# Optimization experiments

Measured on AMD Instinct MI355X. Metric: run time of the kernel, lower is better.

## Reference

```python
import jax, jax.numpy as jnp
import numpy as np

EPS = 1e-5
C = 64  # in_channels == feat_channels == out_channels


def _ln(x, g, b):
    m = jnp.mean(x, axis=-1, keepdims=True)
    v = jnp.mean(jnp.square(x - m), axis=-1, keepdims=True)
    return (x - m) * jax.lax.rsqrt(v + EPS) * g + b


def setup_inputs() -> dict:
    key = jax.random.key(0)
    ks = jax.random.split(key, 10)
    bs, nc, H, W = 8, 80, 256, 256
    d = {
        "feat": jax.random.normal(ks[0], (bs, C, H, W), jnp.float32),
        "head": jax.random.normal(ks[1], (bs, nc, C, 1), jnp.float32),
        "pred": jax.random.normal(ks[2], (bs, nc, H // 2, W // 2), jnp.float32),
        # linear transforms (stored [in, out], applied as x @ W + b)
        "W_pred_t": jax.random.normal(ks[3], (C, 2 * C), jnp.float32) * 0.05,
        "b_pred_t": jnp.zeros((2 * C,), jnp.float32),
        "W_head_t": jax.random.normal(ks[4], (C, 2 * C), jnp.float32) * 0.05,
        "b_head_t": jnp.zeros((2 * C,), jnp.float32),
        "W_pred_g": jax.random.normal(ks[5], (C, C), jnp.float32) * 0.05,
        "b_pred_g": jnp.zeros((C,), jnp.float32),
        "W_head_g": jax.random.normal(ks[6], (C, C), jnp.float32) * 0.05,
        "b_head_g": jnp.zeros((C,), jnp.float32),
        "W_fc": jax.random.normal(ks[7], (C, C), jnp.float32) * 0.05,
        "b_fc": jnp.zeros((C,), jnp.float32),
        # layernorm params
        "g_pin": jnp.ones((C,), jnp.float32), "be_pin": jnp.zeros((C,), jnp.float32),
        "g_hin": jnp.ones((C,), jnp.float32), "be_hin": jnp.zeros((C,), jnp.float32),
        "g_pout": jnp.ones((C,), jnp.float32), "be_pout": jnp.zeros((C,), jnp.float32),
        "g_hout": jnp.ones((C,), jnp.float32), "be_hout": jnp.zeros((C,), jnp.float32),
        "g_fc": jnp.ones((C,), jnp.float32), "be_fc": jnp.zeros((C,), jnp.float32),
    }
    return d


def reference(feat, head, pred,
              W_pred_t, b_pred_t, W_head_t, b_head_t,
              W_pred_g, b_pred_g, W_head_g, b_head_g,
              W_fc, b_fc,
              g_pin, be_pin, g_hin, be_hin,
              g_pout, be_pout, g_hout, be_hout,
              g_fc, be_fc):
    bs, nc = head.shape[:2]
    H, W = feat.shape[2], feat.shape[3]
    pred_up = jax.image.resize(pred, (bs, nc, H, W), method="bilinear")
    pred_up = jax.nn.sigmoid(pred_up)
    # head-aware feature assembly: [bs, nc, C]
    assemble = jnp.einsum("bnhw,bchw->bnc", pred_up, feat)
    a = assemble.reshape(-1, C)                      # [BN, C]
    BN = a.shape[0]
    # head: [bs, nc, C, kk] -> [BN, kk, C]
    hd = jnp.transpose(head.reshape(bs, nc, C, -1), (0, 1, 3, 2)).reshape(BN, -1, C)

    pf = a @ W_pred_t + b_pred_t                     # [BN, 2C]
    pf_in, pf_out = pf[:, :C], pf[:, C:]
    hf = hd @ W_head_t + b_head_t                    # [BN, kk, 2C]
    hf_in, hf_out = hf[..., :C], hf[..., C:]

    gate = hf_in * pf_in[:, None, :]                 # [BN, kk, C]
    head_gate = jax.nn.sigmoid(_ln(gate @ W_head_g + b_head_g, g_hin, be_hin))
    pred_gate = jax.nn.sigmoid(_ln(gate @ W_pred_g + b_pred_g, g_pin, be_pin))

    hf_out = _ln(hf_out, g_hout, be_hout)
    pf_out = _ln(pf_out, g_pout, be_pout)

    upd = pred_gate * pf_out[:, None, :] + head_gate * hf_out
    upd = jax.nn.relu(_ln(upd @ W_fc + b_fc, g_fc, be_fc))
    upd = upd.reshape(bs, nc, -1, C)
    upd = jnp.transpose(upd, (0, 1, 3, 2)).reshape(bs, nc, C, 1, 1)
    return upd
```

## Files before the change

kernel.cpp:

```cpp
#include <hip/hip_runtime.h>
#include <hip/hip_bf16.h>


using bf16x8 = __attribute__((ext_vector_type(8))) short;
using f32x4  = __attribute__((ext_vector_type(4))) float;

#define NPART 64

__device__ __forceinline__ unsigned pk2(float lo, float hi) {
  union { __hip_bfloat162 h2; unsigned u; } cv;
  cv.h2 = __float22bfloat162_rn(make_float2(lo, hi));
  return cv.u;
}
__device__ __forceinline__ float bf2f(unsigned short s) {
  return __uint_as_float(((unsigned)s) << 16);
}

__global__ __launch_bounds__(256) void k_assemble(
    const float* __restrict__ feat, const float* __restrict__ pred,
    float* __restrict__ partial) {
  __shared__ __align__(16) unsigned short yrow[80 * 136];
  __shared__ __align__(16) unsigned short Plds[80 * 264];

  const int tid = threadIdx.x;
  const int b  = blockIdx.x >> 6;
  const int rb = blockIdx.x & 63;
  const int wid = tid >> 6, l = tid & 63;
  const int ch16 = l & 15, kg = l >> 4;
  const int c0 = wid << 4;

  f32x4 acc[5] = {};
  const float* fbase0 = feat + (((size_t)(b * 64 + c0 + ch16)) << 16);

  for (int it = 0; it < 4; ++it) {
    const int h = rb * 4 + it;
    const int p = h & 1, j = h >> 1;
    int r0, r1; float wy0, wy1;
    if (p == 0) { r0 = (j > 0) ? j - 1 : 0; r1 = j; wy0 = 0.25f; wy1 = 0.75f; }
    else        { r0 = j; r1 = (j < 127) ? j + 1 : 127; wy0 = 0.75f; wy1 = 0.25f; }

    #pragma unroll
    for (int i = 0; i < 10; ++i) {
      const int id = tid + 256 * i;
      const int n = id >> 5, cg = id & 31;
      const float* pb = pred + (((size_t)(b * 80 + n)) << 14);
      const float4 v0 = *(const float4*)(pb + (r0 << 7) + cg * 4);
      const float4 v1 = *(const float4*)(pb + (r1 << 7) + cg * 4);
      uint2 s;
      s.x = pk2(wy0 * v0.x + wy1 * v1.x, wy0 * v0.y + wy1 * v1.y);
      s.y = pk2(wy0 * v0.z + wy1 * v1.z, wy0 * v0.w + wy1 * v1.w);
      *(uint2*)&yrow[n * 136 + cg * 4] = s;
    }
    __syncthreads();

    #pragma unroll
    for (int i = 0; i < 10; ++i) {
      const int id = tid + 256 * i;
      const int n = id >> 5, g = id & 31;
      float yv[6];
      #pragma unroll
      for (int k = 0; k < 6; ++k) {
        int col = 4 * g - 1 + k;
        col = col < 0 ? 0 : (col > 127 ? 127 : col);
        yv[k] = bf2f(yrow[n * 136 + col]);
      }
      float P[8];
      #pragma unroll
      for (int px = 0; px < 8; ++px) {
        const int hf = px >> 1;
        float v;
        if ((px & 1) == 0) v = -0.36067376f * yv[hf]     + -1.08202128f * yv[hf + 1];
        else               v = -1.08202128f * yv[hf + 1] + -0.36067376f * yv[hf + 2];
        P[px] = __builtin_amdgcn_rcpf(1.0f + __builtin_amdgcn_exp2f(v));
      }
      uint4 s;
      s.x = pk2(P[0], P[1]); s.y = pk2(P[2], P[3]);
      s.z = pk2(P[4], P[5]); s.w = pk2(P[6], P[7]);
      *(uint4*)&Plds[n * 264 + g * 8] = s;
    }
    __syncthreads();

    const float* fb = fbase0 + h * 256;
    #pragma unroll
    for (int ks = 0; ks < 8; ++ks) {
      const int pw = ks * 32 + kg * 8;
      const float4 f0 = *(const float4*)(fb + pw);
      const float4 f1 = *(const float4*)(fb + pw + 4);
      union { uint4 u; bf16x8 v; } bu;
      bu.u.x = pk2(f0.x, f0.y); bu.u.y = pk2(f0.z, f0.w);
      bu.u.z = pk2(f1.x, f1.y); bu.u.w = pk2(f1.z, f1.w);
      #pragma unroll
      for (int m = 0; m < 5; ++m) {
        const bf16x8 af = *(const bf16x8*)&Plds[(m * 16 + ch16) * 264 + pw];
        acc[m] = __builtin_amdgcn_mfma_f32_16x16x32_bf16(af, bu.v, acc[m], 0, 0, 0);
      }
    }
    __syncthreads();
  }

  float* po = partial + ((size_t)(b * NPART + rb)) * (80 * 64);
  #pragma unroll
  for (int m = 0; m < 5; ++m) {
    #pragma unroll
    for (int q = 0; q < 4; ++q) {
      const int n = m * 16 + kg * 4 + q;
      po[n * 64 + c0 + ch16] = acc[m][q];
    }
  }
}

__device__ __forceinline__ float wred64(float v) {
  #pragma unroll
  for (int off = 32; off > 0; off >>= 1) v += __shfl_xor(v, off, 64);
  return v;
}
__device__ __forceinline__ float lnorm(float x, const float* __restrict__ g,
                                       const float* __restrict__ be, int l) {
  const float m = wred64(x) * 0.015625f;
  const float d = x - m;
  const float var = wred64(d * d) * 0.015625f;
  return d * rsqrtf(var + 1e-5f) * g[l] + be[l];
}
__device__ __forceinline__ float sigmf(float x) {
  return __builtin_amdgcn_rcpf(1.0f + __builtin_amdgcn_exp2f(-1.44269504f * x));
}

__global__ __launch_bounds__(256) void k_head(
    const float* __restrict__ partial, const float* __restrict__ head,
    const float* __restrict__ Wpt, const float* __restrict__ bpt,
    const float* __restrict__ Wht, const float* __restrict__ bht,
    const float* __restrict__ Wpg, const float* __restrict__ bpg,
    const float* __restrict__ Whg, const float* __restrict__ bhg,
    const float* __restrict__ Wfc, const float* __restrict__ bfc,
    const float* __restrict__ g_pin, const float* __restrict__ be_pin,
    const float* __restrict__ g_hin, const float* __restrict__ be_hin,
    const float* __restrict__ g_pout, const float* __restrict__ be_pout,
    const float* __restrict__ g_hout, const float* __restrict__ be_hout,
    const float* __restrict__ g_fc, const float* __restrict__ be_fc,
    float* __restrict__ out) {
  __shared__ float rows[4][4][64];
  const int tid = threadIdx.x, wid = tid >> 6, l = tid & 63;
  const int r = blockIdx.x * 4 + wid;
  const int b = r / 80, n = r % 80;

  const float* pp = partial + (size_t)b * (NPART * 80 * 64) + n * 64 + l;
  float a_c = 0.f;
  #pragma unroll 8
  for (int jj = 0; jj < NPART; ++jj) a_c += pp[(size_t)jj * (80 * 64)];
  rows[wid][0][l] = a_c;
  rows[wid][1][l] = head[(size_t)r * 64 + l];
  __syncthreads();

  float pf_in = bpt[l], pf_out = bpt[64 + l];
  float hf_in = bht[l], hf_out = bht[64 + l];
  #pragma unroll 8
  for (int c = 0; c < 64; ++c) {
    const float av = rows[wid][0][c];
    const float hv = rows[wid][1][c];
    pf_in  += av * Wpt[c * 128 + l];
    pf_out += av * Wpt[c * 128 + 64 + l];
    hf_in  += hv * Wht[c * 128 + l];
    hf_out += hv * Wht[c * 128 + 64 + l];
  }
  const float gate = hf_in * pf_in;
  rows[wid][2][l] = gate;
  __syncthreads();

  float hg = bhg[l], pg = bpg[l];
  #pragma unroll 8
  for (int c = 0; c < 64; ++c) {
    const float gv = rows[wid][2][c];
    hg += gv * Whg[c * 64 + l];
    pg += gv * Wpg[c * 64 + l];
  }
  const float head_gate = sigmf(lnorm(hg, g_hin, be_hin, l));
  const float pred_gate = sigmf(lnorm(pg, g_pin, be_pin, l));
  const float hfo = lnorm(hf_out, g_hout, be_hout, l);
  const float pfo = lnorm(pf_out, g_pout, be_pout, l);
  const float upd = pred_gate * pfo + head_gate * hfo;
  rows[wid][3][l] = upd;
  __syncthreads();

  float fc = bfc[l];
  #pragma unroll 8
  for (int c = 0; c < 64; ++c)
    fc += rows[wid][3][c] * Wfc[c * 64 + l];
  float o = lnorm(fc, g_fc, be_fc, l);
  o = fmaxf(o, 0.f);
  out[(size_t)r * 64 + l] = o;
}

extern "C" void kernel_launch(void* const* d_in, const int* in_sizes, int n_in,
                              void* d_out, int out_size, void* d_ws, size_t ws_size,
                              hipStream_t stream) {
  const float* feat   = (const float*)d_in[0];
  const float* head   = (const float*)d_in[1];
  const float* pred   = (const float*)d_in[2];
  const float* Wpt    = (const float*)d_in[3];
  const float* bpt    = (const float*)d_in[4];
  const float* Wht    = (const float*)d_in[5];
  const float* bht    = (const float*)d_in[6];
  const float* Wpg    = (const float*)d_in[7];
  const float* bpg    = (const float*)d_in[8];
  const float* Whg    = (const float*)d_in[9];
  const float* bhg    = (const float*)d_in[10];
  const float* Wfc    = (const float*)d_in[11];
  const float* bfc    = (const float*)d_in[12];
  const float* g_pin  = (const float*)d_in[13];
  const float* be_pin = (const float*)d_in[14];
  const float* g_hin  = (const float*)d_in[15];
  const float* be_hin = (const float*)d_in[16];
  const float* g_pout = (const float*)d_in[17];
  const float* be_pout= (const float*)d_in[18];
  const float* g_hout = (const float*)d_in[19];
  const float* be_hout= (const float*)d_in[20];
  const float* g_fc   = (const float*)d_in[21];
  const float* be_fc  = (const float*)d_in[22];
  float* out = (float*)d_out;
  float* partial = (float*)d_ws;

  hipLaunchKernelGGL(k_assemble, dim3(8 * NPART), dim3(256), 0, stream,
                     feat, pred, partial);
  hipLaunchKernelGGL(k_head, dim3(160), dim3(256), 0, stream,
                     partial, head, Wpt, bpt, Wht, bht, Wpg, bpg, Whg, bhg,
                     Wfc, bfc, g_pin, be_pin, g_hin, be_hin, g_pout, be_pout,
                     g_hout, be_hout, g_fc, be_fc, out);
}
```

Measured before the change: 64.63 us.

## Prefetch feat tiles into LDS asynchronously with triple buffering, keep upsampled rows in registers

```diff
diff --git a/kernel.cpp b/kernel.cpp
--- a/kernel.cpp
+++ b/kernel.cpp
@@ -5,97 +5,137 @@
 using bf16x8 = __attribute__((ext_vector_type(8))) short;
 using f32x4  = __attribute__((ext_vector_type(4))) float;
 
-#define NPART 64
+#define NPART 32
 
 __device__ __forceinline__ unsigned pk2(float lo, float hi) {
   union { __hip_bfloat162 h2; unsigned u; } cv;
   cv.h2 = __float22bfloat162_rn(make_float2(lo, hi));
   return cv.u;
 }
-__device__ __forceinline__ float bf2f(unsigned short s) {
-  return __uint_as_float(((unsigned)s) << 16);
+__device__ __forceinline__ float sigAB(float a, float b) {
+  return __builtin_amdgcn_rcpf(1.0f + __builtin_amdgcn_exp2f(-0.36067376f * a - 1.08202128f * b));
+}
+__device__ __forceinline__ float sigBA(float a, float b) {
+  return __builtin_amdgcn_rcpf(1.0f + __builtin_amdgcn_exp2f(-1.08202128f * a - 0.36067376f * b));
+}
+
+__device__ __forceinline__ void stage_tile(const float* __restrict__ feat,
+                                           int b, int h, int hf,
+                                           char* ldsbase, int tid) {
+  const int wv = tid >> 6, l = tid & 63;
+  const float* fb = feat + (((size_t)b * 64) << 16) + h * 256 + hf * 128;
+  #pragma unroll
+  for (int i = 0; i < 8; ++i) {
+    const int cid = wv * 8 + i;
+    const int A   = cid * 1024 + l * 16;
+    const int lin = A ^ (((A >> 9) & 7) << 4);
+    const int ch  = lin >> 9;
+    const int px  = (lin & 511) >> 2;
+    const float* src = fb + (((size_t)ch) << 16) + px;
+    __builtin_amdgcn_global_load_lds(
+        (const __attribute__((address_space(1))) void*)src,
+        (__attribute__((address_space(3))) void*)(ldsbase + cid * 1024),
+        16, 0, 0);
+  }
+}
+
+__device__ __forceinline__ void mfma_half(const char* featbuf,
+                                          const unsigned short* Plds,
+                                          int hf, int c0, int ch16, int kg,
+                                          f32x4 acc[5]) {
+  const int ch   = c0 + ch16;
+  const int mask = (ch & 7) << 4;
+  #pragma unroll
+  for (int ks = 0; ks < 4; ++ks) {
+    const int px  = ks * 32 + kg * 8;
+    const int lin = ch * 512 + px * 4;
+    const float4 f0 = *(const float4*)(featbuf + (lin ^ mask));
+    const float4 f1 = *(const float4*)(featbuf + ((lin + 16) ^ mask));
+    union { uint4 u; bf16x8 v; } bu;
+    bu.u.x = pk2(f0.x, f0.y); bu.u.y = pk2(f0.z, f0.w);
+    bu.u.z = pk2(f1.x, f1.y); bu.u.w = pk2(f1.z, f1.w);
+    #pragma unroll
+    for (int m = 0; m < 5; ++m) {
+      const bf16x8 af = *(const bf16x8*)&Plds[(m * 16 + ch16) * 264 + hf * 128 + px];
+      acc[m] = __builtin_amdgcn_mfma_f32_16x16x32_bf16(af, bu.v, acc[m], 0, 0, 0);
+    }
+  }
 }
 
 __global__ __launch_bounds__(256) void k_assemble(
     const float* __restrict__ feat, const float* __restrict__ pred,
     float* __restrict__ partial) {
-  __shared__ __align__(16) unsigned short yrow[80 * 136];
+  __shared__ __align__(16) float FeatLds[3][8192];
   __shared__ __align__(16) unsigned short Plds[80 * 264];
 
   const int tid = threadIdx.x;
-  const int b  = blockIdx.x >> 6;
-  const int rb = blockIdx.x & 63;
+  const int b  = blockIdx.x >> 5;
+  const int rb = blockIdx.x & 31;
   const int wid = tid >> 6, l = tid & 63;
   const int ch16 = l & 15, kg = l >> 4;
   const int c0 = wid << 4;
+  const int h0 = rb * 8;
+  char* fbase = (char*)&FeatLds[0][0];
 
   f32x4 acc[5] = {};
-  const float* fbase0 = feat + (((size_t)(b * 64 + c0 + ch16)) << 16);
-
-  for (int it = 0; it < 4; ++it) {
-    const int h = rb * 4 + it;
-    const int p = h & 1, j = h >> 1;
+
+  stage_tile(feat, b, h0, 0, fbase, tid);
+  stage_tile(feat, b, h0, 1, fbase + 32768, tid);
+
+  const int gg = tid & 31, nb = tid >> 5;
+
+  for (int r = 0; r < 8; ++r) {
+    const int t = 2 * r;
+    const int h = h0 + r;
+    const int j = h >> 1;
     int r0, r1; float wy0, wy1;
-    if (p == 0) { r0 = (j > 0) ? j - 1 : 0; r1 = j; wy0 = 0.25f; wy1 = 0.75f; }
-    else        { r0 = j; r1 = (j < 127) ? j + 1 : 127; wy0 = 0.75f; wy1 = 0.25f; }
-
+    if ((h & 1) == 0) { r0 = (j > 0) ? j - 1 : 0; r1 = j; wy0 = 0.25f; wy1 = 0.75f; }
+    else              { r0 = j; r1 = (j < 127) ? j + 1 : 127; wy0 = 0.75f; wy1 = 0.25f; }
+    float y[10][4];
     #pragma unroll
     for (int i = 0; i < 10; ++i) {
-      const int id = tid + 256 * i;
-      const int n = id >> 5, cg = id & 31;
+      const int n = nb + 8 * i;
       const float* pb = pred + (((size_t)(b * 80 + n)) << 14);
-      const float4 v0 = *(const float4*)(pb + (r0 << 7) + cg * 4);
-      const float4 v1 = *(const float4*)(pb + (r1 << 7) + cg * 4);
-      uint2 s;
-      s.x = pk2(wy0 * v0.x + wy1 * v1.x, wy0 * v0.y + wy1 * v1.y);
-      s.y = pk2(wy0 * v0.z + wy1 * v1.z, wy0 * v0.w + wy1 * v1.w);
-      *(uint2*)&yrow[n * 136 + cg * 4] = s;
+      const float4 v0 = *(const float4*)(pb + (r0 << 7) + gg * 4);
+      const float4 v1 = *(const float4*)(pb + (r1 << 7) + gg * 4);
+      y[i][0] = wy0 * v0.x + wy1 * v1.x; y[i][1] = wy0 * v0.y + wy1 * v1.y;
+      y[i][2] = wy0 * v0.z + wy1 * v1.z; y[i][3] = wy0 * v0.w + wy1 * v1.w;
     }
     __syncthreads();
 
+    if (t + 2 < 16)
+      stage_tile(feat, b, h0 + ((t + 2) >> 1), (t + 2) & 1,
+                 fbase + ((t + 2) % 3) * 32768, tid);
+
     #pragma unroll
     for (int i = 0; i < 10; ++i) {
-      const int id = tid + 256 * i;
-      const int n = id >> 5, g = id & 31;
-      float yv[6];
-      #pragma unroll
-      for (int k = 0; k < 6; ++k) {
-        int col = 4 * g - 1 + k;
-        col = col < 0 ? 0 : (col > 127 ? 127 : col);
-        yv[k] = bf2f(yrow[n * 136 + col]);
-      }
+      const int n = nb + 8 * i;
+      const float y0 = y[i][0], y1 = y[i][1], y2 = y[i][2], y3 = y[i][3];
+      float yl = __shfl_up(y3, 1, 64);  if (gg == 0)  yl = y0;
+      float yr = __shfl_down(y0, 1, 64); if (gg == 31) yr = y3;
       float P[8];
-      #pragma unroll
-      for (int px = 0; px < 8; ++px) {
-        const int hf = px >> 1;
-        float v;
-        if ((px & 1) == 0) v = -0.36067376f * yv[hf]     + -1.08202128f * yv[hf + 1];
-        else               v = -1.08202128f * yv[hf + 1] + -0.36067376f * yv[hf + 2];
-        P[px] = __builtin_amdgcn_rcpf(1.0f + __builtin_amdgcn_exp2f(v));
-      }
+      P[0] = sigAB(yl, y0); P[1] = sigBA(y0, y1);
+      P[2] = sigAB(y0, y1); P[3] = sigBA(y1, y2);
+      P[4] = sigAB(y1, y2); P[5] = sigBA(y2, y3);
+      P[6] = sigAB(y2, y3); P[7] = sigBA(y3, yr);
       uint4 s;
       s.x = pk2(P[0], P[1]); s.y = pk2(P[2], P[3]);
       s.z = pk2(P[4], P[5]); s.w = pk2(P[6], P[7]);
-      *(uint4*)&Plds[n * 264 + g * 8] = s;
-    }
-    __syncthreads();
-
-    const float* fb = fbase0 + h * 256;
-    #pragma unroll
-    for (int ks = 0; ks < 8; ++ks) {
-      const int pw = ks * 32 + kg * 8;
-      const float4 f0 = *(const float4*)(fb + pw);
-      const float4 f1 = *(const float4*)(fb + pw + 4);
-      union { uint4 u; bf16x8 v; } bu;
-      bu.u.x = pk2(f0.x, f0.y); bu.u.y = pk2(f0.z, f0.w);
-      bu.u.z = pk2(f1.x, f1.y); bu.u.w = pk2(f1.z, f1.w);
-      #pragma unroll
-      for (int m = 0; m < 5; ++m) {
-        const bf16x8 af = *(const bf16x8*)&Plds[(m * 16 + ch16) * 264 + pw];
-        acc[m] = __builtin_amdgcn_mfma_f32_16x16x32_bf16(af, bu.v, acc[m], 0, 0, 0);
-      }
-    }
-    __syncthreads();
+      *(uint4*)&Plds[n * 264 + gg * 8] = s;
+    }
+    asm volatile("s_waitcnt lgkmcnt(0)" ::: "memory");
+    __builtin_amdgcn_s_barrier();
+
+    mfma_half(fbase + (t % 3) * 32768, Plds, 0, c0, ch16, kg, acc);
+
+    asm volatile("s_waitcnt lgkmcnt(0)" ::: "memory");
+    __builtin_amdgcn_s_barrier();
+
+    if (t + 3 < 16)
+      stage_tile(feat, b, h0 + ((t + 3) >> 1), (t + 3) & 1,
+                 fbase + ((t + 3) % 3) * 32768, tid);
+
+    mfma_half(fbase + ((t + 1) % 3) * 32768, Plds, 1, c0, ch16, kg, acc);
   }
 
   float* po = partial + ((size_t)(b * NPART + rb)) * (80 * 64);
```

Result: slower. 70.18 us (+8.6%).

## Register-prefetch pred rows, shuffle-based horizontal interp, swizzled fragment LDS layout

Applied to the files above, without the earlier changes.

```diff
diff --git a/kernel.cpp b/kernel.cpp
--- a/kernel.cpp
+++ b/kernel.cpp
@@ -12,15 +12,17 @@
   cv.h2 = __float22bfloat162_rn(make_float2(lo, hi));
   return cv.u;
 }
-__device__ __forceinline__ float bf2f(unsigned short s) {
-  return __uint_as_float(((unsigned)s) << 16);
-}
-
-__global__ __launch_bounds__(256) void k_assemble(
+__device__ __forceinline__ float sigAB(float a, float b) {
+  return __builtin_amdgcn_rcpf(1.0f + __builtin_amdgcn_exp2f(-0.36067376f * a - 1.08202128f * b));
+}
+__device__ __forceinline__ float sigBA(float a, float b) {
+  return __builtin_amdgcn_rcpf(1.0f + __builtin_amdgcn_exp2f(-1.08202128f * a - 0.36067376f * b));
+}
+
+__global__ __launch_bounds__(256, 2) void k_assemble(
     const float* __restrict__ feat, const float* __restrict__ pred,
     float* __restrict__ partial) {
-  __shared__ __align__(16) unsigned short yrow[80 * 136];
-  __shared__ __align__(16) unsigned short Plds[80 * 264];
+  __shared__ __align__(16) unsigned short Pfrag[40 * 64 * 8];
 
   const int tid = threadIdx.x;
   const int b  = blockIdx.x >> 6;
@@ -28,70 +30,89 @@
   const int wid = tid >> 6, l = tid & 63;
   const int ch16 = l & 15, kg = l >> 4;
   const int c0 = wid << 4;
+  const int h0 = rb * 4;
+  const int gg = tid & 31, nb = tid >> 5;
 
   f32x4 acc[5] = {};
-  const float* fbase0 = feat + (((size_t)(b * 64 + c0 + ch16)) << 16);
-
-  for (int it = 0; it < 4; ++it) {
-    const int h = rb * 4 + it;
-    const int p = h & 1, j = h >> 1;
-    int r0, r1; float wy0, wy1;
-    if (p == 0) { r0 = (j > 0) ? j - 1 : 0; r1 = j; wy0 = 0.25f; wy1 = 0.75f; }
-    else        { r0 = j; r1 = (j < 127) ? j + 1 : 127; wy0 = 0.75f; wy1 = 0.25f; }
-
+
+  const float* fwave = feat + (((size_t)(b * 64 + c0 + ch16)) << 16);
+  const float* pbat  = pred + (((size_t)(b * 80)) << 14);
+
+  float4 p0[10], p1[10];
+
+  {
+    const int j = h0 >> 1;
+    const int r0 = (j > 0) ? j - 1 : 0, r1 = j;
     #pragma unroll
     for (int i = 0; i < 10; ++i) {
-      const int id = tid + 256 * i;
-      const int n = id >> 5, cg = id & 31;
-      const float* pb = pred + (((size_t)(b * 80 + n)) << 14);
-      const float4 v0 = *(const float4*)(pb + (r0 << 7) + cg * 4);
-      const float4 v1 = *(const float4*)(pb + (r1 << 7) + cg * 4);
-      uint2 s;
-      s.x = pk2(wy0 * v0.x + wy1 * v1.x, wy0 * v0.y + wy1 * v1.y);
-      s.y = pk2(wy0 * v0.z + wy1 * v1.z, wy0 * v0.w + wy1 * v1.w);
-      *(uint2*)&yrow[n * 136 + cg * 4] = s;
-    }
-    __syncthreads();
+      const int n = nb + 8 * i;
+      const float* pb = pbat + (((size_t)n) << 14);
+      p0[i] = *(const float4*)(pb + (r0 << 7) + gg * 4);
+      p1[i] = *(const float4*)(pb + (r1 << 7) + gg * 4);
+    }
+  }
+
+  #pragma unroll
+  for (int r = 0; r < 4; ++r) {
+    const int h = h0 + r;
+    const float wy0 = (r & 1) ? 0.75f : 0.25f;
+    const float wy1 = (r & 1) ? 0.25f : 0.75f;
 
     #pragma unroll
     for (int i = 0; i < 10; ++i) {
-      const int id = tid + 256 * i;
-      const int n = id >> 5, g = id & 31;
-      float yv[6];
-      #pragma unroll
-      for (int k = 0; k < 6; ++k) {
-        int col = 4 * g - 1 + k;
-        col = col < 0 ? 0 : (col > 127 ? 127 : col);
-        yv[k] = bf2f(yrow[n * 136 + col]);
-      }
+      const int n = nb + 8 * i;
+      const float y0 = wy0 * p0[i].x + wy1 * p1[i].x;
+      const float y1 = wy0 * p0[i].y + wy1 * p1[i].y;
+      const float y2 = wy0 * p0[i].z + wy1 * p1[i].z;
+      const float y3 = wy0 * p0[i].w + wy1 * p1[i].w;
+      float yl = __shfl_up(y3, 1, 64);   if (gg == 0)  yl = y0;
+      float yr = __shfl_down(y0, 1, 64); if (gg == 31) yr = y3;
       float P[8];
-      #pragma unroll
-      for (int px = 0; px < 8; ++px) {
-        const int hf = px >> 1;
-        float v;
-        if ((px & 1) == 0) v = -0.36067376f * yv[hf]     + -1.08202128f * yv[hf + 1];
-        else               v = -1.08202128f * yv[hf + 1] + -0.36067376f * yv[hf + 2];
-        P[px] = __builtin_amdgcn_rcpf(1.0f + __builtin_amdgcn_exp2f(v));
-      }
+      P[0] = sigAB(yl, y0); P[1] = sigBA(y0, y1);
+      P[2] = sigAB(y0, y1); P[3] = sigBA(y1, y2);
+      P[4] = sigAB(y1, y2); P[5] = sigBA(y2, y3);
+      P[6] = sigAB(y2, y3); P[7] = sigBA(y3, yr);
       uint4 s;
       s.x = pk2(P[0], P[1]); s.y = pk2(P[2], P[3]);
       s.z = pk2(P[4], P[5]); s.w = pk2(P[6], P[7]);
-      *(uint4*)&Plds[n * 264 + g * 8] = s;
+      const int ks = gg >> 2, kgw = gg & 3;
+      const int slot = kgw * 16 + ((n & 15) ^ ks);
+      *(uint4*)&Pfrag[(((ks * 5 + (n >> 4)) * 64) + slot) * 8] = s;
     }
     __syncthreads();
 
-    const float* fb = fbase0 + h * 256;
+    const float* fb = fwave + h * 256;
+    float4 f[16];
     #pragma unroll
     for (int ks = 0; ks < 8; ++ks) {
       const int pw = ks * 32 + kg * 8;
-      const float4 f0 = *(const float4*)(fb + pw);
-      const float4 f1 = *(const float4*)(fb + pw + 4);
+      f[2 * ks]     = *(const float4*)(fb + pw);
+      f[2 * ks + 1] = *(const float4*)(fb + pw + 4);
+    }
+    if (r < 3) {
+      const int hn = h + 1;
+      const int j = hn >> 1;
+      int r0, r1;
+      if ((hn & 1) == 0) { r0 = (j > 0) ? j - 1 : 0; r1 = j; }
+      else               { r0 = j; r1 = (j < 127) ? j + 1 : 127; }
+      #pragma unroll
+      for (int i = 0; i < 10; ++i) {
+        const int n = nb + 8 * i;
+        const float* pb = pbat + (((size_t)n) << 14);
+        p0[i] = *(const float4*)(pb + (r0 << 7) + gg * 4);
+        p1[i] = *(const float4*)(pb + (r1 << 7) + gg * 4);
+      }
+    }
+    #pragma unroll
+    for (int ks = 0; ks < 8; ++ks) {
+      const float4 f0 = f[2 * ks], f1 = f[2 * ks + 1];
       union { uint4 u; bf16x8 v; } bu;
       bu.u.x = pk2(f0.x, f0.y); bu.u.y = pk2(f0.z, f0.w);
       bu.u.z = pk2(f1.x, f1.y); bu.u.w = pk2(f1.z, f1.w);
+      const int slot = kg * 16 + (ch16 ^ ks);
       #pragma unroll
       for (int m = 0; m < 5; ++m) {
-        const bf16x8 af = *(const bf16x8*)&Plds[(m * 16 + ch16) * 264 + pw];
+        const bf16x8 af = *(const bf16x8*)&Pfrag[(((ks * 5 + m) * 64) + slot) * 8];
         acc[m] = __builtin_amdgcn_mfma_f32_16x16x32_bf16(af, bu.v, acc[m], 0, 0, 0);
       }
     }
```

After: 64.28 us. Within noise of the previous version (-0.5%).
